# Kernel tuning notes

Measured on AMD Instinct MI355X. Metric: run time of the kernel, lower is better.

Reference implementation:

```python
import jax, jax.numpy as jnp
import numpy as np

NUM_HEADS = 8

def setup_inputs() -> dict:
    key = jax.random.key(0)
    k1, k2, k3, k4, k5 = jax.random.split(key, 5)
    B, N, C = 4, 2048, 512
    x = jax.random.normal(k1, (B, N, C), dtype=jnp.float32)
    s = 1.0 / np.sqrt(C)
    qkv_w = jax.random.uniform(k2, (3 * C, C), dtype=jnp.float32, minval=-s, maxval=s)
    qkv_b = jax.random.uniform(k3, (3 * C,), dtype=jnp.float32, minval=-s, maxval=s)
    proj_w = jax.random.uniform(k4, (C, C), dtype=jnp.float32, minval=-s, maxval=s)
    proj_b = jax.random.uniform(k5, (C,), dtype=jnp.float32, minval=-s, maxval=s)
    return {"x": x, "qkv_w": qkv_w, "qkv_b": qkv_b, "proj_w": proj_w, "proj_b": proj_b}

def reference(x, qkv_w, qkv_b, proj_w, proj_b):
    B, N, C = x.shape
    H = NUM_HEADS
    D = C // H
    scale = D ** -0.5
    # qkv: [B,N,3C] -> [3,B,H,N,D]
    qkv = (jnp.einsum('bnc,oc->bno', x, qkv_w) + qkv_b)
    qkv = qkv.reshape(B, N, 3, H, D).transpose(2, 0, 3, 1, 4)
    q, k, v = qkv[0], qkv[1], qkv[2]
    attn = jnp.einsum('bhnd,bhmd->bhnm', q, k) * scale  # [B,H,N,N]
    attn = jax.nn.softmax(attn, axis=-1)
    out = jnp.einsum('bhnm,bhmd->bhnd', attn, v)  # [B,H,N,D]
    out = out.transpose(0, 2, 1, 3).reshape(B, N, C)
    return jnp.einsum('bnc,oc->bno', out, proj_w) + proj_b
```

## Files before the change

### kernel.cpp

```cpp
#include <hip/hip_runtime.h>
#include <stdint.h>


typedef short bf16x8 __attribute__((ext_vector_type(8)));
typedef float f32x4  __attribute__((ext_vector_type(4)));
typedef float f32x16 __attribute__((ext_vector_type(16)));
typedef unsigned int u32x4 __attribute__((ext_vector_type(4)));

__device__ __forceinline__ unsigned short f2bf(float f) {
    unsigned int u = __builtin_bit_cast(unsigned int, f);
    u += 0x7fffu + ((u >> 16) & 1u);
    return (unsigned short)(u >> 16);
}
__device__ __forceinline__ unsigned int pk2(float a, float b) {
    return (unsigned int)f2bf(a) | ((unsigned int)f2bf(b) << 16);
}
__device__ __forceinline__ float fexp2(float x) {
    return __builtin_amdgcn_exp2f(x);
}
__device__ __forceinline__ bf16x8 ld8_f32(const float* __restrict__ p) {
    float4 f0 = *(const float4*)p;
    float4 f1 = *(const float4*)(p + 4);
    u32x4 u = {pk2(f0.x, f0.y), pk2(f0.z, f0.w), pk2(f1.x, f1.y), pk2(f1.z, f1.w)};
    return __builtin_bit_cast(bf16x8, u);
}
__device__ __forceinline__ void async16(const void* g, void* l) {
    __builtin_amdgcn_global_load_lds(
        (const __attribute__((address_space(1))) unsigned int*)g,
        (__attribute__((address_space(3))) unsigned int*)l,
        16, 0, 0);
}

#define MFMA16(a, b, c) __builtin_amdgcn_mfma_f32_16x16x32_bf16((a), (b), (c), 0, 0, 0)
#define MFMA32(a, b, c) __builtin_amdgcn_mfma_f32_32x32x16_bf16((a), (b), (c), 0, 0, 0)

__global__ void cvt_bf16(const float* __restrict__ x,
                         const float* __restrict__ w,
                         unsigned short* __restrict__ xb,
                         unsigned short* __restrict__ wb)
{
    const int G = 524288 + 98304;
    for (int idx = blockIdx.x * 256 + threadIdx.x; idx < G; idx += gridDim.x * 256) {
        if (idx < 524288)
            *(bf16x8*)(xb + (size_t)idx * 8) = ld8_f32(x + (size_t)idx * 8);
        else {
            int j = idx - 524288;
            *(bf16x8*)(wb + (size_t)j * 8) = ld8_f32(w + (size_t)j * 8);
        }
    }
}
__global__ void cvt_w2(const float* __restrict__ w, unsigned short* __restrict__ wb)
{
    int idx = blockIdx.x * 256 + threadIdx.x;
    *(bf16x8*)(wb + (size_t)idx * 8) = ld8_f32(w + (size_t)idx * 8);
}

template <int MODE>
__global__ __launch_bounds__(256, 2)
void gemm_bt(const unsigned short* __restrict__ A,
             const unsigned short* __restrict__ B,
             const float* __restrict__ bias,
             unsigned short* __restrict__ out0,
             unsigned short* __restrict__ out1,
             unsigned short* __restrict__ out2,
             float* __restrict__ outf,
             int K, int N)
{
    __shared__ unsigned short sA[128 * 32];
    __shared__ unsigned short sB[128 * 32];

    const int tid  = threadIdx.x;
    const int wave = tid >> 6, lane = tid & 63;
    const int l = lane & 15, q16 = lane >> 4;
    const int wm = wave >> 1, wn = wave & 1;
    const int m0 = blockIdx.y * 128;
    const int n0 = blockIdx.x * 128;

    f32x4 acc[4][4];
#pragma unroll
    for (int i = 0; i < 4; ++i)
#pragma unroll
        for (int j = 0; j < 4; ++j)
            acc[i][j] = (f32x4){0.f, 0.f, 0.f, 0.f};

    for (int k0 = 0; k0 < K; k0 += 32) {
#pragma unroll
        for (int call = 0; call < 2; ++call) {
            int L = call * 256 + tid;
            int r = L >> 2, c = L & 3;
            async16(A + (size_t)(m0 + r) * K + k0 + c * 8, sA + L * 8);
            async16(B + (size_t)(n0 + r) * K + k0 + c * 8, sB + L * 8);
        }
        __syncthreads();

        bf16x8 af[4], bfr[4];
#pragma unroll
        for (int i = 0; i < 4; ++i) {
            int row = wm * 64 + i * 16 + l;
            af[i] = *(const bf16x8*)(sA + (row * 4 + q16) * 8);
        }
#pragma unroll
        for (int j = 0; j < 4; ++j) {
            int row = wn * 64 + j * 16 + l;
            bfr[j] = *(const bf16x8*)(sB + (row * 4 + q16) * 8);
        }
#pragma unroll
        for (int i = 0; i < 4; ++i)
#pragma unroll
            for (int j = 0; j < 4; ++j)
                acc[i][j] = MFMA16(af[i], bfr[j], acc[i][j]);
        __syncthreads();
    }

    const float lscale = 0.18033688f;
#pragma unroll
    for (int i = 0; i < 4; ++i) {
#pragma unroll
        for (int j = 0; j < 4; ++j) {
            int col = n0 + wn * 64 + j * 16 + l;
            float bv = bias[col];
#pragma unroll
            for (int r = 0; r < 4; ++r) {
                int row = m0 + wm * 64 + i * 16 + q16 * 4 + r;
                float val = acc[i][j][r] + bv;
                if (MODE == 0) {
                    int which = col >> 9;
                    int h = (col >> 6) & 7, d = col & 63;
                    int b = row >> 11, n = row & 2047;
                    if (which == 0)
                        out0[(size_t)(((b * 8 + h) * 2048) + n) * 64 + d] = f2bf(val * lscale);
                    else if (which == 1)
                        out1[(size_t)(((b * 8 + h) * 2048) + n) * 64 + d] = f2bf(val);
                    else
                        out2[(size_t)(((b * 8 + h) * 64) + d) * 2048 + n] = f2bf(val);
                } else {
                    outf[(size_t)row * N + col] = val;
                }
            }
        }
    }
}

__global__ __launch_bounds__(256, 2)
void attn_fused(const unsigned short* __restrict__ Q,
                const unsigned short* __restrict__ Km,
                const unsigned short* __restrict__ Vt,
                unsigned short* __restrict__ O)
{
    __shared__ unsigned short sK[2][128 * 64];
    __shared__ unsigned short sVt[2][64 * 128];

    const int tid  = threadIdx.x;
    const int wave = tid >> 6, lane = tid & 63;
    const int l31 = lane & 31, h = lane >> 5;
    const int bh = blockIdx.y;
    const int n0 = blockIdx.x * 128;
    const int q0 = n0 + wave * 32;

    const size_t kbase = (size_t)bh * 2048 * 64;
    const size_t vbase = (size_t)bh * 64 * 2048;

    bf16x8 qf[4];
#pragma unroll
    for (int ks = 0; ks < 4; ++ks)
        qf[ks] = *(const bf16x8*)(Q + (size_t)(bh * 2048 + q0 + l31) * 64 + ks * 16 + h * 8);

    f32x16 oacc[2];
#pragma unroll
    for (int dt = 0; dt < 2; ++dt)
#pragma unroll
        for (int e = 0; e < 16; ++e) oacc[dt][e] = 0.f;
    float m_run = -1e30f, l_run = 0.f;

    auto stage = [&](int buf, int kv) {
#pragma unroll
        for (int call = 0; call < 4; ++call) {
            int s = wave * 256 + call * 64 + lane;
            int rk = s >> 3, ck = (s & 7) ^ (rk & 7);
            async16(Km + kbase + (size_t)(kv + rk) * 64 + ck * 8, &sK[buf][s * 8]);
            int rv = s >> 4, cv = (s & 15) ^ (rv & 7);
            async16(Vt + vbase + (size_t)rv * 2048 + kv + cv * 8, &sVt[buf][s * 8]);
        }
    };

    stage(0, 0);
    __syncthreads();

    for (int it = 0; it < 16; ++it) {
        const int cur = it & 1;
        if (it < 15) stage(cur ^ 1, (it + 1) * 128);

        f32x16 sacc[4];
#pragma unroll
        for (int mt = 0; mt < 4; ++mt) {
#pragma unroll
            for (int e = 0; e < 16; ++e) sacc[mt][e] = 0.f;
            const int rk = mt * 32 + l31;
#pragma unroll
            for (int ks = 0; ks < 4; ++ks) {
                int c = ks * 2 + h;
                bf16x8 kf = *(const bf16x8*)(&sK[cur][(rk * 8 + (c ^ (rk & 7))) * 8]);
                sacc[mt] = MFMA32(kf, qf[ks], sacc[mt]);
            }
        }

        float mx = -1e30f;
#pragma unroll
        for (int mt = 0; mt < 4; ++mt)
#pragma unroll
            for (int e = 0; e < 16; ++e) mx = fmaxf(mx, sacc[mt][e]);
        mx = fmaxf(mx, __shfl_xor(mx, 32));
        float mn = fmaxf(m_run, mx);
        if (__any((mn > m_run) ? 1 : 0)) {
            float a = fexp2(m_run - mn);
            m_run = mn;
            l_run *= a;
#pragma unroll
            for (int dt = 0; dt < 2; ++dt)
#pragma unroll
                for (int e = 0; e < 16; ++e) oacc[dt][e] *= a;
        }
        float rs = 0.f;
        unsigned int pk[4][4][2];
#pragma unroll
        for (int mt = 0; mt < 4; ++mt)
#pragma unroll
            for (int g = 0; g < 4; ++g) {
                unsigned int u0 = __builtin_bit_cast(unsigned int, fexp2(sacc[mt][4 * g + 0] - mn));
                unsigned int u1 = __builtin_bit_cast(unsigned int, fexp2(sacc[mt][4 * g + 1] - mn));
                unsigned int u2 = __builtin_bit_cast(unsigned int, fexp2(sacc[mt][4 * g + 2] - mn));
                unsigned int u3 = __builtin_bit_cast(unsigned int, fexp2(sacc[mt][4 * g + 3] - mn));
                unsigned int t0 = u0 & 0xffff0000u, t1 = u1 & 0xffff0000u;
                unsigned int t2 = u2 & 0xffff0000u, t3 = u3 & 0xffff0000u;
                rs += (__builtin_bit_cast(float, t0) + __builtin_bit_cast(float, t1))
                    + (__builtin_bit_cast(float, t2) + __builtin_bit_cast(float, t3));
                pk[mt][g][0] = (u0 >> 16) | t1;
                pk[mt][g][1] = (u2 >> 16) | t3;
            }
        rs += __shfl_xor(rs, 32);
        l_run += rs;

#pragma unroll
        for (int mt = 0; mt < 4; ++mt) {
#pragma unroll
            for (int ks2 = 0; ks2 < 2; ++ks2) {
                unsigned int send0 = h ? pk[mt][2 * ks2][0] : pk[mt][2 * ks2 + 1][0];
                unsigned int send1 = h ? pk[mt][2 * ks2][1] : pk[mt][2 * ks2 + 1][1];
                unsigned int rcv0 = __shfl_xor(send0, 32);
                unsigned int rcv1 = __shfl_xor(send1, 32);
                unsigned int own0 = h ? pk[mt][2 * ks2 + 1][0] : pk[mt][2 * ks2][0];
                unsigned int own1 = h ? pk[mt][2 * ks2 + 1][1] : pk[mt][2 * ks2][1];
                u32x4 bu;
                bu[0] = h ? rcv0 : own0;
                bu[1] = h ? rcv1 : own1;
                bu[2] = h ? own0 : rcv0;
                bu[3] = h ? own1 : rcv1;
                bf16x8 bfrag = __builtin_bit_cast(bf16x8, bu);
                int c = mt * 4 + ks2 * 2 + h;
#pragma unroll
                for (int dt = 0; dt < 2; ++dt) {
                    int rv = dt * 32 + l31;
                    bf16x8 vf = *(const bf16x8*)(&sVt[cur][(rv * 16 + (c ^ (rv & 7))) * 8]);
                    oacc[dt] = MFMA32(vf, bfrag, oacc[dt]);
                }
            }
        }
        __syncthreads();
    }

    const int b = bh >> 3, hh = bh & 7;
    float inv = 1.f / fmaxf(l_run, 1e-20f);
    unsigned short* obase = O + ((size_t)(b * 2048 + q0 + l31)) * 512 + hh * 64;
#pragma unroll
    for (int dt = 0; dt < 2; ++dt)
#pragma unroll
        for (int g = 0; g < 4; ++g) {
            int d = dt * 32 + 8 * g + 4 * h;
            unsigned int w0 = pk2(oacc[dt][4 * g + 0] * inv, oacc[dt][4 * g + 1] * inv);
            unsigned int w1 = pk2(oacc[dt][4 * g + 2] * inv, oacc[dt][4 * g + 3] * inv);
            uint2 w = {w0, w1};
            *(uint2*)(obase + d) = w;
        }
}

extern "C" void kernel_launch(void* const* d_in, const int* in_sizes, int n_in,
                              void* d_out, int out_size, void* d_ws, size_t ws_size,
                              hipStream_t stream)
{
    const float* x      = (const float*)d_in[0];
    const float* qkv_w  = (const float*)d_in[1];
    const float* qkv_b  = (const float*)d_in[2];
    const float* proj_w = (const float*)d_in[3];
    const float* proj_b = (const float*)d_in[4];

    const size_t PER = 4u * 8u * 2048u * 64u;
    unsigned short* q_ws  = (unsigned short*)d_ws;
    unsigned short* k_ws  = q_ws  + PER;
    unsigned short* vt_ws = k_ws  + PER;
    unsigned short* ao_ws = vt_ws + PER;

    unsigned short* xb = (unsigned short*)d_out;
    unsigned short* wb = xb + PER;

    cvt_bf16<<<dim3(640), 256, 0, stream>>>(x, qkv_w, xb, wb);
    gemm_bt<0><<<dim3(12, 64), 256, 0, stream>>>(
        xb, wb, qkv_b, q_ws, k_ws, vt_ws, nullptr, 512, 1536);
    attn_fused<<<dim3(16, 32), 256, 0, stream>>>(q_ws, k_ws, vt_ws, ao_ws);
    cvt_w2<<<dim3(128), 256, 0, stream>>>(proj_w, k_ws);
    gemm_bt<1><<<dim3(4, 64), 256, 0, stream>>>(
        ao_ws, k_ws, proj_b, nullptr, nullptr, nullptr, (float*)d_out, 512, 512);
}
```

Measured before the change: 176.6 us.

## Split GEMM kernels, shrink output-projection tile, precompute attention addresses and stagger prefetch

The templated GEMM is split into a QKV kernel and an output-projection kernel. The projection now uses 64-row tiles, so it launches twice as many blocks and fills more of the GPU. The attention kernel precomputes swizzled LDS and global offsets and splits the K and V prefetch so V is issued after the QK MFMAs. It also always rescales the accumulator instead of branching on a wave vote, and packs bf16 probabilities with a byte permute. The softmax row sum now uses full-precision probabilities rather than the bf16-truncated values fed to the MFMA. Unconditional rescaling adds ALU work on tiles where the running max does not change.

```diff
diff --git a/kernel.cpp b/kernel.cpp
--- a/kernel.cpp
+++ b/kernel.cpp
@@ -55,16 +55,14 @@
     *(bf16x8*)(wb + (size_t)idx * 8) = ld8_f32(w + (size_t)idx * 8);
 }
 
-template <int MODE>
 __global__ __launch_bounds__(256, 2)
-void gemm_bt(const unsigned short* __restrict__ A,
-             const unsigned short* __restrict__ B,
-             const float* __restrict__ bias,
-             unsigned short* __restrict__ out0,
-             unsigned short* __restrict__ out1,
-             unsigned short* __restrict__ out2,
-             float* __restrict__ outf,
-             int K, int N)
+void gemm_qkv(const unsigned short* __restrict__ A,
+              const unsigned short* __restrict__ B,
+              const float* __restrict__ bias,
+              unsigned short* __restrict__ out0,
+              unsigned short* __restrict__ out1,
+              unsigned short* __restrict__ out2,
+              int K)
 {
     __shared__ unsigned short sA[128 * 32];
     __shared__ unsigned short sB[128 * 32];
@@ -95,15 +93,11 @@
 
         bf16x8 af[4], bfr[4];
 #pragma unroll
-        for (int i = 0; i < 4; ++i) {
-            int row = wm * 64 + i * 16 + l;
-            af[i] = *(const bf16x8*)(sA + (row * 4 + q16) * 8);
-        }
-#pragma unroll
-        for (int j = 0; j < 4; ++j) {
-            int row = wn * 64 + j * 16 + l;
-            bfr[j] = *(const bf16x8*)(sB + (row * 4 + q16) * 8);
-        }
+        for (int i = 0; i < 4; ++i)
+            af[i] = *(const bf16x8*)(sA + ((wm * 64 + i * 16 + l) * 4 + q16) * 8);
+#pragma unroll
+        for (int j = 0; j < 4; ++j)
+            bfr[j] = *(const bf16x8*)(sB + ((wn * 64 + j * 16 + l) * 4 + q16) * 8);
 #pragma unroll
         for (int i = 0; i < 4; ++i)
 #pragma unroll
@@ -123,19 +117,82 @@
             for (int r = 0; r < 4; ++r) {
                 int row = m0 + wm * 64 + i * 16 + q16 * 4 + r;
                 float val = acc[i][j][r] + bv;
-                if (MODE == 0) {
-                    int which = col >> 9;
-                    int h = (col >> 6) & 7, d = col & 63;
-                    int b = row >> 11, n = row & 2047;
-                    if (which == 0)
-                        out0[(size_t)(((b * 8 + h) * 2048) + n) * 64 + d] = f2bf(val * lscale);
-                    else if (which == 1)
-                        out1[(size_t)(((b * 8 + h) * 2048) + n) * 64 + d] = f2bf(val);
-                    else
-                        out2[(size_t)(((b * 8 + h) * 64) + d) * 2048 + n] = f2bf(val);
-                } else {
-                    outf[(size_t)row * N + col] = val;
-                }
+                int which = col >> 9;
+                int h = (col >> 6) & 7, d = col & 63;
+                int b = row >> 11, n = row & 2047;
+                if (which == 0)
+                    out0[(size_t)(((b * 8 + h) * 2048) + n) * 64 + d] = f2bf(val * lscale);
+                else if (which == 1)
+                    out1[(size_t)(((b * 8 + h) * 2048) + n) * 64 + d] = f2bf(val);
+                else
+                    out2[(size_t)(((b * 8 + h) * 64) + d) * 2048 + n] = f2bf(val);
+            }
+        }
+    }
+}
+
+__global__ __launch_bounds__(256, 2)
+void gemm_out(const unsigned short* __restrict__ A,
+              const unsigned short* __restrict__ B,
+              const float* __restrict__ bias,
+              float* __restrict__ outf,
+              int K, int N)
+{
+    __shared__ unsigned short sA[64 * 32];
+    __shared__ unsigned short sB[128 * 32];
+
+    const int tid  = threadIdx.x;
+    const int wave = tid >> 6, lane = tid & 63;
+    const int l = lane & 15, q16 = lane >> 4;
+    const int wm = wave >> 1, wn = wave & 1;
+    const int m0 = blockIdx.y * 64;
+    const int n0 = blockIdx.x * 128;
+
+    f32x4 acc[2][4];
+#pragma unroll
+    for (int i = 0; i < 2; ++i)
+#pragma unroll
+        for (int j = 0; j < 4; ++j)
+            acc[i][j] = (f32x4){0.f, 0.f, 0.f, 0.f};
+
+    for (int k0 = 0; k0 < K; k0 += 32) {
+        {
+            int r = tid >> 2, c = tid & 3;
+            async16(A + (size_t)(m0 + r) * K + k0 + c * 8, sA + tid * 8);
+        }
+#pragma unroll
+        for (int call = 0; call < 2; ++call) {
+            int L = call * 256 + tid;
+            int r = L >> 2, c = L & 3;
+            async16(B + (size_t)(n0 + r) * K + k0 + c * 8, sB + L * 8);
+        }
+        __syncthreads();
+
+        bf16x8 af[2], bfr[4];
+#pragma unroll
+        for (int i = 0; i < 2; ++i)
+            af[i] = *(const bf16x8*)(sA + ((wm * 32 + i * 16 + l) * 4 + q16) * 8);
+#pragma unroll
+        for (int j = 0; j < 4; ++j)
+            bfr[j] = *(const bf16x8*)(sB + ((wn * 64 + j * 16 + l) * 4 + q16) * 8);
+#pragma unroll
+        for (int i = 0; i < 2; ++i)
+#pragma unroll
+            for (int j = 0; j < 4; ++j)
+                acc[i][j] = MFMA16(af[i], bfr[j], acc[i][j]);
+        __syncthreads();
+    }
+
+#pragma unroll
+    for (int i = 0; i < 2; ++i) {
+#pragma unroll
+        for (int j = 0; j < 4; ++j) {
+            int col = n0 + wn * 64 + j * 16 + l;
+            float bv = bias[col];
+#pragma unroll
+            for (int r = 0; r < 4; ++r) {
+                int row = m0 + wm * 32 + i * 16 + q16 * 4 + r;
+                outf[(size_t)row * N + col] = acc[i][j][r] + bv;
             }
         }
     }
@@ -153,12 +210,36 @@
     const int tid  = threadIdx.x;
     const int wave = tid >> 6, lane = tid & 63;
     const int l31 = lane & 31, h = lane >> 5;
+    const int swz = l31 & 7;
     const int bh = blockIdx.y;
     const int n0 = blockIdx.x * 128;
     const int q0 = n0 + wave * 32;
 
-    const size_t kbase = (size_t)bh * 2048 * 64;
-    const size_t vbase = (size_t)bh * 64 * 2048;
+    const unsigned short* Kp = Km + (size_t)bh * 2048 * 64;
+    const unsigned short* Vp = Vt + (size_t)bh * 64 * 2048;
+    const unsigned short* sKf = &sK[0][0];
+    const unsigned short* sVf = &sVt[0][0];
+
+    int ka[4], va[2][2];
+#pragma unroll
+    for (int ks = 0; ks < 4; ++ks)
+        ka[ks] = l31 * 64 + ((ks * 2 + h) ^ swz) * 8;
+#pragma unroll
+    for (int m1 = 0; m1 < 2; ++m1)
+#pragma unroll
+        for (int ks2 = 0; ks2 < 2; ++ks2)
+            va[m1][ks2] = l31 * 128 + ((m1 * 4 + ks2 * 2 + h) ^ swz) * 8;
+
+    int ksrc[4], vsrc[4], dst[4];
+#pragma unroll
+    for (int c = 0; c < 4; ++c) {
+        int s = wave * 256 + c * 64 + lane;
+        int rk = s >> 3;
+        ksrc[c] = rk * 64 + ((s & 7) ^ (rk & 7)) * 8;
+        int rv = s >> 4;
+        vsrc[c] = rv * 2048 + ((s & 15) ^ (rv & 7)) * 8;
+        dst[c] = s * 8;
+    }
 
     bf16x8 qf[4];
 #pragma unroll
@@ -172,36 +253,39 @@
         for (int e = 0; e < 16; ++e) oacc[dt][e] = 0.f;
     float m_run = -1e30f, l_run = 0.f;
 
-    auto stage = [&](int buf, int kv) {
-#pragma unroll
-        for (int call = 0; call < 4; ++call) {
-            int s = wave * 256 + call * 64 + lane;
-            int rk = s >> 3, ck = (s & 7) ^ (rk & 7);
-            async16(Km + kbase + (size_t)(kv + rk) * 64 + ck * 8, &sK[buf][s * 8]);
-            int rv = s >> 4, cv = (s & 15) ^ (rv & 7);
-            async16(Vt + vbase + (size_t)rv * 2048 + kv + cv * 8, &sVt[buf][s * 8]);
-        }
-    };
-
-    stage(0, 0);
+#pragma unroll
+    for (int c = 0; c < 4; ++c) {
+        async16(Kp + ksrc[c], (void*)(sKf + dst[c]));
+        async16(Vp + vsrc[c], (void*)(sVf + dst[c]));
+    }
     __syncthreads();
 
     for (int it = 0; it < 16; ++it) {
-        const int cur = it & 1;
-        if (it < 15) stage(cur ^ 1, (it + 1) * 128);
+        const int nb = ((it + 1) & 1) * 8192;
+        if (it < 15) {
+            int kv = (it + 1) * 128;
+#pragma unroll
+            for (int c = 0; c < 4; ++c)
+                async16(Kp + (size_t)kv * 64 + ksrc[c], (void*)(sKf + nb + dst[c]));
+        }
 
         f32x16 sacc[4];
 #pragma unroll
         for (int mt = 0; mt < 4; ++mt) {
 #pragma unroll
             for (int e = 0; e < 16; ++e) sacc[mt][e] = 0.f;
-            const int rk = mt * 32 + l31;
 #pragma unroll
             for (int ks = 0; ks < 4; ++ks) {
-                int c = ks * 2 + h;
-                bf16x8 kf = *(const bf16x8*)(&sK[cur][(rk * 8 + (c ^ (rk & 7))) * 8]);
+                bf16x8 kf = *(const bf16x8*)(sKf + ka[ks] + mt * 2048);
                 sacc[mt] = MFMA32(kf, qf[ks], sacc[mt]);
             }
+        }
+
+        if (it < 15) {
+            int kv = (it + 1) * 128;
+#pragma unroll
+            for (int c = 0; c < 4; ++c)
+                async16(Vp + (size_t)kv + vsrc[c], (void*)(sVf + nb + dst[c]));
         }
 
         float mx = -1e30f;
@@ -211,31 +295,31 @@
             for (int e = 0; e < 16; ++e) mx = fmaxf(mx, sacc[mt][e]);
         mx = fmaxf(mx, __shfl_xor(mx, 32));
         float mn = fmaxf(m_run, mx);
-        if (__any((mn > m_run) ? 1 : 0)) {
-            float a = fexp2(m_run - mn);
-            m_run = mn;
-            l_run *= a;
-#pragma unroll
-            for (int dt = 0; dt < 2; ++dt)
-#pragma unroll
-                for (int e = 0; e < 16; ++e) oacc[dt][e] *= a;
-        }
+        float a = fexp2(m_run - mn);
+        m_run = mn;
+        l_run *= a;
+#pragma unroll
+        for (int dt = 0; dt < 2; ++dt)
+#pragma unroll
+            for (int e = 0; e < 16; ++e) oacc[dt][e] *= a;
+
         float rs = 0.f;
         unsigned int pk[4][4][2];
 #pragma unroll
         for (int mt = 0; mt < 4; ++mt)
 #pragma unroll
             for (int g = 0; g < 4; ++g) {
-                unsigned int u0 = __builtin_bit_cast(unsigned int, fexp2(sacc[mt][4 * g + 0] - mn));
-                unsigned int u1 = __builtin_bit_cast(unsigned int, fexp2(sacc[mt][4 * g + 1] - mn));
-                unsigned int u2 = __builtin_bit_cast(unsigned int, fexp2(sacc[mt][4 * g + 2] - mn));
-                unsigned int u3 = __builtin_bit_cast(unsigned int, fexp2(sacc[mt][4 * g + 3] - mn));
-                unsigned int t0 = u0 & 0xffff0000u, t1 = u1 & 0xffff0000u;
-                unsigned int t2 = u2 & 0xffff0000u, t3 = u3 & 0xffff0000u;
-                rs += (__builtin_bit_cast(float, t0) + __builtin_bit_cast(float, t1))
-                    + (__builtin_bit_cast(float, t2) + __builtin_bit_cast(float, t3));
-                pk[mt][g][0] = (u0 >> 16) | t1;
-                pk[mt][g][1] = (u2 >> 16) | t3;
+                float p0 = fexp2(sacc[mt][4 * g + 0] - mn);
+                float p1 = fexp2(sacc[mt][4 * g + 1] - mn);
+                float p2 = fexp2(sacc[mt][4 * g + 2] - mn);
+                float p3 = fexp2(sacc[mt][4 * g + 3] - mn);
+                rs += (p0 + p1) + (p2 + p3);
+                pk[mt][g][0] = __builtin_amdgcn_perm(
+                    __builtin_bit_cast(unsigned int, p1),
+                    __builtin_bit_cast(unsigned int, p0), 0x07060302u);
+                pk[mt][g][1] = __builtin_amdgcn_perm(
+                    __builtin_bit_cast(unsigned int, p3),
+                    __builtin_bit_cast(unsigned int, p2), 0x07060302u);
             }
         rs += __shfl_xor(rs, 32);
         l_run += rs;
@@ -256,15 +340,18 @@
                 bu[2] = h ? own0 : rcv0;
                 bu[3] = h ? own1 : rcv1;
                 bf16x8 bfrag = __builtin_bit_cast(bf16x8, bu);
-                int c = mt * 4 + ks2 * 2 + h;
 #pragma unroll
                 for (int dt = 0; dt < 2; ++dt) {
-                    int rv = dt * 32 + l31;
-                    bf16x8 vf = *(const bf16x8*)(&sVt[cur][(rv * 16 + (c ^ (rv & 7))) * 8]);
+                    bf16x8 vf = *(const bf16x8*)(sVf + va[mt & 1][ks2]
+                                                 + (mt >> 1) * 64 + dt * 4096);
                     oacc[dt] = MFMA32(vf, bfrag, oacc[dt]);
                 }
             }
         }
+
+#pragma unroll
+        for (int ks = 0; ks < 4; ++ks) ka[ks] ^= 8192;
+        va[0][0] ^= 8192; va[0][1] ^= 8192; va[1][0] ^= 8192; va[1][1] ^= 8192;
         __syncthreads();
     }
 
@@ -303,10 +390,8 @@
     unsigned short* wb = xb + PER;
 
     cvt_bf16<<<dim3(640), 256, 0, stream>>>(x, qkv_w, xb, wb);
-    gemm_bt<0><<<dim3(12, 64), 256, 0, stream>>>(
-        xb, wb, qkv_b, q_ws, k_ws, vt_ws, nullptr, 512, 1536);
+    gemm_qkv<<<dim3(12, 64), 256, 0, stream>>>(xb, wb, qkv_b, q_ws, k_ws, vt_ws, 512);
     attn_fused<<<dim3(16, 32), 256, 0, stream>>>(q_ws, k_ws, vt_ws, ao_ws);
     cvt_w2<<<dim3(128), 256, 0, stream>>>(proj_w, k_ws);
-    gemm_bt<1><<<dim3(4, 64), 256, 0, stream>>>(
-        ao_ws, k_ws, proj_b, nullptr, nullptr, nullptr, (float*)d_out, 512, 512);
-}
+    gemm_out<<<dim3(4, 128), 256, 0, stream>>>(ao_ws, k_ws, proj_b, (float*)d_out, 512, 512);
+}
```

Result: faster. 172.4 us (-2.4%).
